# Performance work log

Measured on AMD Instinct MI355X. Metric: run time of the kernel, lower is better.

The kernel has to match this reference:

```python
import jax, jax.numpy as jnp
import numpy as np

B = 2048          # batch
K = 32            # max active features per side
NF = 22528        # feature_set.num_features
L1 = 2048
L2 = 16
L3 = 32
P = 8             # num_psqt_buckets
NLS = 8           # num_ls_buckets
QP = 255.0        # 8-bit unsigned LSQ upper bound


def setup_inputs() -> dict:
    key = jax.random.key(0)
    ks = jax.random.split(key, 16)
    us = jax.random.bernoulli(ks[0], 0.5, (B, 1)).astype(jnp.float32)
    them = 1.0 - us
    white_indices = jax.random.randint(ks[1], (B, K), 0, NF)
    black_indices = jax.random.randint(ks[2], (B, K), 0, NF)
    white_values = jnp.ones((B, K), jnp.float32)
    black_values = jnp.ones((B, K), jnp.float32)
    psqt_indices = jax.random.randint(ks[3], (B,), 0, P)
    layer_stack_indices = jax.random.randint(ks[4], (B,), 0, NLS)
    # parameters
    ft_weight = jax.random.normal(ks[5], (NF, L1 + P), jnp.float32) * 0.01
    ft_bias = jax.random.normal(ks[6], (L1 + P,), jnp.float32) * 0.01
    lsq_s = jnp.full((4,), 1.0 / 128.0, jnp.float32)  # per-group step size
    W1 = jax.random.normal(ks[7], (NLS, L2, L1), jnp.float32) * (1.0 / np.sqrt(L1))
    b1 = jnp.zeros((NLS, L2), jnp.float32)
    W2 = jax.random.normal(ks[8], (NLS, L3, L2), jnp.float32) * (1.0 / np.sqrt(L2))
    b2 = jnp.zeros((NLS, L3), jnp.float32)
    Wo = jax.random.normal(ks[9], (NLS, 1, L3), jnp.float32) * (1.0 / np.sqrt(L3))
    bo = jnp.zeros((NLS, 1), jnp.float32)
    return dict(us=us, them=them, white_indices=white_indices, white_values=white_values,
                black_indices=black_indices, black_values=black_values,
                psqt_indices=psqt_indices, layer_stack_indices=layer_stack_indices,
                ft_weight=ft_weight, ft_bias=ft_bias, lsq_s=lsq_s,
                W1=W1, b1=b1, W2=W2, b2=b2, Wo=Wo, bo=bo)


def _feature_transform(idx, val, ft_weight, ft_bias):
    # sparse accumulation: sum_k val[b,k] * ft_weight[idx[b,k], :]
    emb = ft_weight[idx]                           # [B, K, L1+P]
    return jnp.einsum('bk,bkd->bd', val, emb) + ft_bias


def _lsq(x, s):
    # LSQ activation, 4 groups over feature dim, 8-bit unsigned, STE round
    b, d = x.shape
    g = x.reshape(b, 4, d // 4) / s[None, :, None]
    gc = jnp.clip(g, 0.0, QP)
    gq = gc + jax.lax.stop_gradient(jnp.round(gc) - gc)
    return (gq * s[None, :, None]).reshape(b, d)


def reference(us, them, white_indices, white_values, black_indices, black_values,
              psqt_indices, layer_stack_indices,
              ft_weight, ft_bias, lsq_s, W1, b1, W2, b2, Wo, bo):
    wp = _feature_transform(white_indices, white_values, ft_weight, ft_bias)
    bp = _feature_transform(black_indices, black_values, ft_weight, ft_bias)
    w, wpsqt = wp[:, :L1], wp[:, L1:]
    b, bpsqt = bp[:, :L1], bp[:, L1:]
    l0 = us * jnp.concatenate([w, b], axis=1) + them * jnp.concatenate([b, w], axis=1)
    l0q = _lsq(l0, lsq_s)                          # [B, 2*L1]
    s0, s1, s2, s3 = jnp.split(l0q, 4, axis=1)
    l0_mixed = jnp.concatenate([s0 * s1, s2 * s3], axis=1)   # [B, L1]
    # psqt bucket gather
    wps = jnp.take_along_axis(wpsqt, psqt_indices[:, None], axis=1)  # [B,1]
    bps = jnp.take_along_axis(bpsqt, psqt_indices[:, None], axis=1)
    # per-sample layer-stack (expert) selection
    i = layer_stack_indices
    h1 = jnp.clip(jnp.einsum('bi,boi->bo', l0_mixed, W1[i]) + b1[i], 0.0, 1.0)
    h2 = jnp.clip(jnp.einsum('bi,boi->bo', h1, W2[i]) + b2[i], 0.0, 1.0)
    ls_out = jnp.einsum('bi,boi->bo', h2, Wo[i]) + bo[i]     # [B,1]
    return ls_out + (wps - bps) * (us - 0.5)
```

## Files before the change

### kernel.cpp

```cpp
#include <hip/hip_runtime.h>

#define BB 2048
#define K 32
#define ROW 2056
#define L1D 2048
#define NFEAT 22528

typedef unsigned short us8 __attribute__((ext_vector_type(8)));
typedef signed char    c8  __attribute__((ext_vector_type(8)));
typedef signed char    c16 __attribute__((ext_vector_type(16)));
typedef float          f8  __attribute__((ext_vector_type(8)));

#define S_T   (0.0625f / 128.0f)
#define INV_S (128.0f / 0.0625f)

#define TBLC_BYTES ((size_t)NFEAT * 2048)
#define W1_ELEMS   ((size_t)8 * 16 * L1D)
#define W1_OFF     TBLC_BYTES
#define PSQ_OFF    (W1_OFF + W1_ELEMS * 2)
#define WS_NEEDED  (PSQ_OFF + (size_t)NFEAT * 8 * 4)

#define TBL_N8 (NFEAT * 256)
#define W1_N8  ((int)(W1_ELEMS / 8))
#define CONV_N (TBL_N8 + W1_N8 + NFEAT)

__device__ __forceinline__ float bf2f(unsigned short s) {
    union { unsigned int u; float f; } v; v.u = ((unsigned int)s) << 16; return v.f;
}

__device__ __forceinline__ unsigned short f2bf(float f) {
    union { float f; unsigned int u; } v; v.f = f;
    const unsigned int u = v.u;
    return (unsigned short)((u + 0x7fffu + ((u >> 16) & 1u)) >> 16);
}

__device__ __forceinline__ signed char f2i8(float f) {
    return (signed char)(int)rintf(fminf(fmaxf(f * INV_S, -127.f), 127.f));
}

__device__ __forceinline__ void fma4(float4& a, float v, const float4 t) {
    a.x = fmaf(v, t.x, a.x); a.y = fmaf(v, t.y, a.y);
    a.z = fmaf(v, t.z, a.z); a.w = fmaf(v, t.w, a.w);
}

__device__ __forceinline__ float4 add4(float4 a, float4 b) {
    float4 r; r.x = a.x + b.x; r.y = a.y + b.y; r.z = a.z + b.z; r.w = a.w + b.w;
    return r;
}

__device__ __forceinline__ float4 mix4(float ua, float4 a, float ub, float4 b) {
    float4 r;
    r.x = fmaf(ua, a.x, ub * b.x); r.y = fmaf(ua, a.y, ub * b.y);
    r.z = fmaf(ua, a.z, ub * b.z); r.w = fmaf(ua, a.w, ub * b.w);
    return r;
}

__device__ __forceinline__ float lsq1(float g, float s) {
    return rintf(fminf(fmaxf(g / s, 0.f), 255.f)) * s;
}

__device__ __forceinline__ float4 lsq4(float4 g, float s) {
    float4 r;
    r.x = lsq1(g.x, s); r.y = lsq1(g.y, s); r.z = lsq1(g.z, s); r.w = lsq1(g.w, s);
    return r;
}

__device__ __forceinline__ float4 mul4(float4 a, float4 b) {
    float4 r; r.x = a.x * b.x; r.y = a.y * b.y; r.z = a.z * b.z; r.w = a.w * b.w;
    return r;
}

__global__ __launch_bounds__(256) void conv_all(const float* __restrict__ ftw,
                                                const float* __restrict__ W1,
                                                signed char* __restrict__ tblc,
                                                unsigned short* __restrict__ w1bf,
                                                float* __restrict__ psqtc) {
    int i = blockIdx.x * blockDim.x + threadIdx.x;
    const int stride = gridDim.x * blockDim.x;
    for (; i < CONV_N; i += stride) {
        if (i < TBL_N8) {
            const int row = i >> 8, c = i & 255;
            const float* src = ftw + (size_t)row * ROW + c * 8;
            const float4 a = ((const float4*)src)[0];
            const float4 b = ((const float4*)src)[1];
            c8 o;
            o[0] = f2i8(a.x); o[1] = f2i8(a.y); o[2] = f2i8(a.z); o[3] = f2i8(a.w);
            o[4] = f2i8(b.x); o[5] = f2i8(b.y); o[6] = f2i8(b.z); o[7] = f2i8(b.w);
            *(c8*)(tblc + ((size_t)row << 11) + c * 8) = o;
        } else if (i < TBL_N8 + W1_N8) {
            const int j = i - TBL_N8;
            const float* src = W1 + (size_t)j * 8;
            const float4 a = ((const float4*)src)[0];
            const float4 b = ((const float4*)src)[1];
            us8 o;
            o[0] = f2bf(a.x); o[1] = f2bf(a.y); o[2] = f2bf(a.z); o[3] = f2bf(a.w);
            o[4] = f2bf(b.x); o[5] = f2bf(b.y); o[6] = f2bf(b.z); o[7] = f2bf(b.w);
            *(us8*)(w1bf + (size_t)j * 8) = o;
        } else {
            const int r = i - TBL_N8 - W1_N8;
            const float4* src = (const float4*)(ftw + (size_t)r * ROW + 2048);
            float4* dst = (float4*)(psqtc + (size_t)r * 8);
            dst[0] = src[0]; dst[1] = src[1];
        }
    }
}

struct __align__(32) SBuf {
    float aw[2048];
    float ab[2048];
    float h1t[16];
    float h1[16];
    float h2[32];
    float psq;
};

__global__ __launch_bounds__(256, 4) void nnue_main2(
    const float* __restrict__ us_p, const float* __restrict__ them_p,
    const int* __restrict__ widx, const float* __restrict__ wval,
    const int* __restrict__ bidx, const float* __restrict__ bval,
    const int* __restrict__ psqt_idx, const int* __restrict__ ls_idx,
    const float* __restrict__ ftb, const float* __restrict__ lsq_s,
    const signed char* __restrict__ tblc, const unsigned short* __restrict__ w1bf,
    const float* __restrict__ psqtc,
    const float* __restrict__ b1, const float* __restrict__ W2,
    const float* __restrict__ b2, const float* __restrict__ Wo,
    const float* __restrict__ bo, float* __restrict__ out)
{
    __shared__ SBuf sb;
    const int b = blockIdx.x;
    const int t = threadIdx.x;

    const float usv = us_p[b];
    const float thv = them_p[b];

    const int side = t >> 7;
    const int tc   = t & 127;
    const int*   idxp = side ? bidx : widx;
    const float* valp = side ? bval : wval;
    const int kb = b * K;

    float acc[16];
    #pragma unroll
    for (int j = 0; j < 16; ++j) acc[j] = 0.f;

    c16 buf[8];
    #pragma unroll
    for (int p = 0; p < 8; ++p)
        buf[p] = ((const c16*)(tblc + ((size_t)idxp[kb + p] << 11)))[tc];
    #pragma unroll
    for (int k = 0; k < K; ++k) {
        const c16 l = buf[k & 7];
        if (k + 8 < K)
            buf[k & 7] = ((const c16*)(tblc + ((size_t)idxp[kb + k + 8] << 11)))[tc];
        const float v = valp[kb + k];
        #pragma unroll
        for (int j = 0; j < 16; ++j) acc[j] = fmaf(v, (float)l[j], acc[j]);
    }

    {
        float* dst = (side ? sb.ab : sb.aw) + 16 * tc;
        const float* fb = ftb + 16 * tc;
        #pragma unroll
        for (int j = 0; j < 16; ++j) dst[j] = fmaf(acc[j], S_T, fb[j]);
    }

    const int pi = psqt_idx[b];
    if (t < 64) {
        const int k = t & 31;
        const int   idx = (t < 32) ? widx[kb + k] : bidx[kb + k];
        const float val = (t < 32) ? wval[kb + k] : bval[kb + k];
        float c = val * psqtc[(size_t)idx * 8 + pi];
        c += __shfl_down(c, 16, 32); c += __shfl_down(c, 8, 32);
        c += __shfl_down(c, 4, 32);  c += __shfl_down(c, 2, 32);
        c += __shfl_down(c, 1, 32);
        const float bsum = __shfl(c, 32);
        if (t == 0) sb.psq = (c - bsum) * (usv - 0.5f);
    }
    __syncthreads();

    {
        const float s0 = lsq_s[0], s1 = lsq_s[1], s2 = lsq_s[2], s3 = lsq_s[3];
        const f8 aw = ((const f8*)sb.aw)[t];
        const f8 ab = ((const f8*)sb.ab)[t];
        const float sA = (t < 128) ? s0 : s1;
        const float sB = (t < 128) ? s2 : s3;
        f8 qa, qb;
        #pragma unroll
        for (int j = 0; j < 8; ++j) {
            qa[j] = lsq1(fmaf(usv, aw[j], thv * ab[j]), sA);
            qb[j] = lsq1(fmaf(usv, ab[j], thv * aw[j]), sB);
        }
        ((f8*)sb.aw)[t] = qa;
        ((f8*)sb.ab)[t] = qb;
    }
    __syncthreads();

    if (t < 128) {
        const f8 x = ((const f8*)sb.aw)[t];
        const f8 y = ((const f8*)sb.aw)[t + 128];
        ((f8*)sb.aw)[t] = x * y;
    } else {
        const f8 x = ((const f8*)sb.ab)[t - 128];
        const f8 y = ((const f8*)sb.ab)[t];
        ((f8*)sb.ab)[t - 128] = x * y;
    }
    __syncthreads();

    const int i = ls_idx[b];
    {
        const int o   = t >> 4;
        const int sub = t & 15;
        const us8* Wrow = (const us8*)(w1bf + (((size_t)i * 16 + o) << 11));
        f8 a8 = (f8)0.f;
        #pragma unroll
        for (int jj = 0; jj < 8; ++jj) {
            const int c = sub + (jj << 4);
            const f8 m = ((const f8*)sb.aw)[c];
            const us8 w = Wrow[c];
            #pragma unroll
            for (int j = 0; j < 8; ++j) a8[j] = fmaf(m[j], bf2f(w[j]), a8[j]);
        }
        #pragma unroll
        for (int jj = 8; jj < 16; ++jj) {
            const int c = sub + ((jj - 8) << 4);
            const f8 m = ((const f8*)sb.ab)[c];
            const us8 w = Wrow[sub + (jj << 4)];
            #pragma unroll
            for (int j = 0; j < 8; ++j) a8[j] = fmaf(m[j], bf2f(w[j]), a8[j]);
        }
        float acc1 = ((a8[0]+a8[1]) + (a8[2]+a8[3])) + ((a8[4]+a8[5]) + (a8[6]+a8[7]));
        acc1 += __shfl_down(acc1, 8, 16); acc1 += __shfl_down(acc1, 4, 16);
        acc1 += __shfl_down(acc1, 2, 16); acc1 += __shfl_down(acc1, 1, 16);
        if (sub == 0) sb.h1t[o] = acc1;
    }
    __syncthreads();

    if (t < 16) {
        const float v = sb.h1t[t] + b1[i * 16 + t];
        sb.h1[t] = fminf(fmaxf(v, 0.f), 1.f);
    }
    __syncthreads();

    if (t < 32) {
        const float* W2i = W2 + (size_t)i * 32 * 16 + t * 16;
        float v = b2[i * 32 + t];
        #pragma unroll
        for (int j = 0; j < 16; ++j) v = fmaf(sb.h1[j], W2i[j], v);
        sb.h2[t] = fminf(fmaxf(v, 0.f), 1.f);
    }
    __syncthreads();

    if (t == 0) {
        const float* Woi = Wo + (size_t)i * 32;
        float v = bo[i];
        #pragma unroll
        for (int j = 0; j < 32; ++j) v = fmaf(sb.h2[j], Woi[j], v);
        out[b] = v + sb.psq;
    }
}

__global__ __launch_bounds__(512, 4) void nnue_fwd_f32(
    const float* __restrict__ us_p, const float* __restrict__ them_p,
    const int* __restrict__ widx, const float* __restrict__ wval,
    const int* __restrict__ bidx, const float* __restrict__ bval,
    const int* __restrict__ psqt_idx, const int* __restrict__ ls_idx,
    const float* __restrict__ ftw, const float* __restrict__ ftb,
    const float* __restrict__ lsq_s, const float* __restrict__ W1,
    const float* __restrict__ b1, const float* __restrict__ W2,
    const float* __restrict__ b2, const float* __restrict__ Wo,
    const float* __restrict__ bo, float* __restrict__ out)
{
    const int b = blockIdx.x;
    const int t = threadIdx.x;
    __shared__ float4 sQA[512]; __shared__ float4 sQB[512]; __shared__ float4 sMx[512];
    __shared__ float sH1t[16]; __shared__ float sH1[16]; __shared__ float sH2[32];
    __shared__ float sPsq;
    const float usv = us_p[b]; const float thv = them_p[b];
    float4 aw = {0,0,0,0}, ab = {0,0,0,0};
    #pragma unroll 4
    for (int k = 0; k < K; ++k) {
        const int iw = widx[b*K+k]; const float vw = wval[b*K+k];
        const int ibx = bidx[b*K+k]; const float vb = bval[b*K+k];
        fma4(aw, vw, ((const float4*)(ftw + (size_t)iw * ROW))[t]);
        fma4(ab, vb, ((const float4*)(ftw + (size_t)ibx * ROW))[t]);
    }
    const int pi = psqt_idx[b];
    if (t < 64) {
        const int k = t & 31;
        const int   idx = (t < 32) ? widx[b*K+k] : bidx[b*K+k];
        const float val = (t < 32) ? wval[b*K+k] : bval[b*K+k];
        float cc = val * ftw[(size_t)idx * ROW + 2048 + pi];
        cc += __shfl_down(cc, 16, 32); cc += __shfl_down(cc, 8, 32);
        cc += __shfl_down(cc, 4, 32); cc += __shfl_down(cc, 2, 32); cc += __shfl_down(cc, 1, 32);
        const float bsum = __shfl(cc, 32);
        if (t == 0) sPsq = (cc - bsum) * (usv - 0.5f);
    }
    const float s0 = lsq_s[0], s1 = lsq_s[1], s2 = lsq_s[2], s3 = lsq_s[3];
    const float4 bias = ((const float4*)ftb)[t];
    aw = add4(aw, bias); ab = add4(ab, bias);
    const float sA = (t < 256) ? s0 : s1;
    const float sB = (t < 256) ? s2 : s3;
    sQA[t] = lsq4(mix4(usv, aw, thv, ab), sA);
    sQB[t] = lsq4(mix4(usv, ab, thv, aw), sB);
    __syncthreads();
    if (t < 256) { sMx[t] = mul4(sQA[t], sQA[t+256]); sMx[t+256] = mul4(sQB[t], sQB[t+256]); }
    __syncthreads();
    const int i = ls_idx[b];
    const float* W1i = W1 + (size_t)i * 16 * L1D;
    {
        const int o = t >> 5; const int sub = t & 31;
        const float4* Wrow = (const float4*)(W1i + o * L1D);
        float4 a4 = {0,0,0,0};
        #pragma unroll
        for (int jj = 0; jj < 16; ++jj) {
            const int j4 = sub + (jj << 5);
            const float4 m = sMx[j4]; const float4 w = Wrow[j4];
            a4.x = fmaf(m.x, w.x, a4.x); a4.y = fmaf(m.y, w.y, a4.y);
            a4.z = fmaf(m.z, w.z, a4.z); a4.w = fmaf(m.w, w.w, a4.w);
        }
        float acc = (a4.x + a4.y) + (a4.z + a4.w);
        acc += __shfl_down(acc, 16, 32); acc += __shfl_down(acc, 8, 32);
        acc += __shfl_down(acc, 4, 32); acc += __shfl_down(acc, 2, 32); acc += __shfl_down(acc, 1, 32);
        if (sub == 0) sH1t[o] = acc;
    }
    __syncthreads();
    if (t < 16) sH1[t] = fminf(fmaxf(sH1t[t] + b1[i*16+t], 0.f), 1.f);
    __syncthreads();
    if (t < 32) {
        const float* W2i = W2 + (size_t)i * 32 * 16 + t * 16;
        float v = b2[i*32+t];
        #pragma unroll
        for (int j = 0; j < 16; ++j) v = fmaf(sH1[j], W2i[j], v);
        sH2[t] = fminf(fmaxf(v, 0.f), 1.f);
    }
    __syncthreads();
    if (t == 0) {
        const float* Woi = Wo + (size_t)i * 32;
        float v = bo[i];
        #pragma unroll
        for (int j = 0; j < 32; ++j) v = fmaf(sH2[j], Woi[j], v);
        out[b] = v + sPsq;
    }
}

extern "C" void kernel_launch(void* const* d_in, const int* in_sizes, int n_in,
                              void* d_out, int out_size, void* d_ws, size_t ws_size,
                              hipStream_t stream) {
    const float* us_p  = (const float*)d_in[0];
    const float* them  = (const float*)d_in[1];
    const int*   widx  = (const int*)d_in[2];
    const float* wval  = (const float*)d_in[3];
    const int*   bidx  = (const int*)d_in[4];
    const float* bval  = (const float*)d_in[5];
    const int*   pidx  = (const int*)d_in[6];
    const int*   lidx  = (const int*)d_in[7];
    const float* ftw   = (const float*)d_in[8];
    const float* ftb   = (const float*)d_in[9];
    const float* lsqs  = (const float*)d_in[10];
    const float* W1    = (const float*)d_in[11];
    const float* b1    = (const float*)d_in[12];
    const float* W2    = (const float*)d_in[13];
    const float* b2    = (const float*)d_in[14];
    const float* Wo    = (const float*)d_in[15];
    const float* bo    = (const float*)d_in[16];
    float* out = (float*)d_out;

    if (ws_size >= WS_NEEDED) {
        signed char*    tblc  = (signed char*)d_ws;
        unsigned short* w1bf  = (unsigned short*)((char*)d_ws + W1_OFF);
        float*          psqtc = (float*)((char*)d_ws + PSQ_OFF);
        conv_all<<<dim3(8192), dim3(256), 0, stream>>>(ftw, W1, tblc, w1bf, psqtc);
        nnue_main2<<<dim3(BB), dim3(256), 0, stream>>>(
            us_p, them, widx, wval, bidx, bval, pidx, lidx,
            ftb, lsqs, tblc, w1bf, psqtc, b1, W2, b2, Wo, bo, out);
    } else {
        nnue_fwd_f32<<<dim3(BB), dim3(512), 0, stream>>>(
            us_p, them, widx, wval, bidx, bval, pidx, lidx,
            ftw, ftb, lsqs, W1, b1, W2, b2, Wo, bo, out);
    }
}
```

Baseline: 338.5 us.

## Split feature gather into column-tiled kernel with transposed int8 table

The int8 feature table is re-laid out as 16 column tiles of 128 bytes per feature. A new gather kernel assigns blocks to (tile, sample chunk) pairs, so each block touches only one 2.9 MB tile slice, which aims to improve cache locality of the random row gathers. The accumulators go through global fp32 scratch (2×16 MB) and are read back by a second kernel that does bias, LSQ and the layer stack. This adds an extra kernel launch and round-trip global traffic in exchange for the better gather locality.

```diff
diff --git a/kernel.cpp b/kernel.cpp
--- a/kernel.cpp
+++ b/kernel.cpp
@@ -5,6 +5,8 @@
 #define ROW 2056
 #define L1D 2048
 #define NFEAT 22528
+#define NTILE 16
+#define TCOLS 128
 
 typedef unsigned short us8 __attribute__((ext_vector_type(8)));
 typedef signed char    c8  __attribute__((ext_vector_type(8)));
@@ -14,15 +16,17 @@
 #define S_T   (0.0625f / 128.0f)
 #define INV_S (128.0f / 0.0625f)
 
-#define TBLC_BYTES ((size_t)NFEAT * 2048)
+#define TBLT_BYTES ((size_t)NFEAT * 2048)
 #define W1_ELEMS   ((size_t)8 * 16 * L1D)
-#define W1_OFF     TBLC_BYTES
+#define W1_OFF     TBLT_BYTES
 #define PSQ_OFF    (W1_OFF + W1_ELEMS * 2)
-#define WS_NEEDED  (PSQ_OFF + (size_t)NFEAT * 8 * 4)
-
-#define TBL_N8 (NFEAT * 256)
-#define W1_N8  ((int)(W1_ELEMS / 8))
-#define CONV_N (TBL_N8 + W1_N8 + NFEAT)
+#define ACCW_OFF   (PSQ_OFF + (size_t)NFEAT * 8 * 4)
+#define ACCB_OFF   (ACCW_OFF + (size_t)BB * L1D * 4)
+#define WS_NEEDED  (ACCB_OFF + (size_t)BB * L1D * 4)
+
+#define TBL_N8  (NFEAT * 256)
+#define W1_N8   ((int)(W1_ELEMS / 8))
+#define CONV_N  (TBL_N8 + W1_N8 + NFEAT)
 
 __device__ __forceinline__ float bf2f(unsigned short s) {
     union { unsigned int u; float f; } v; v.u = ((unsigned int)s) << 16; return v.f;
@@ -72,7 +76,7 @@
 
 __global__ __launch_bounds__(256) void conv_all(const float* __restrict__ ftw,
                                                 const float* __restrict__ W1,
-                                                signed char* __restrict__ tblc,
+                                                signed char* __restrict__ tblT,
                                                 unsigned short* __restrict__ w1bf,
                                                 float* __restrict__ psqtc) {
     int i = blockIdx.x * blockDim.x + threadIdx.x;
@@ -86,7 +90,8 @@
             c8 o;
             o[0] = f2i8(a.x); o[1] = f2i8(a.y); o[2] = f2i8(a.z); o[3] = f2i8(a.w);
             o[4] = f2i8(b.x); o[5] = f2i8(b.y); o[6] = f2i8(b.z); o[7] = f2i8(b.w);
-            *(c8*)(tblc + ((size_t)row << 11) + c * 8) = o;
+            signed char* dst = tblT + ((size_t)(c >> 4) * NFEAT + row) * TCOLS + (c & 15) * 8;
+            *(c8*)dst = o;
         } else if (i < TBL_N8 + W1_N8) {
             const int j = i - TBL_N8;
             const float* src = W1 + (size_t)j * 8;
@@ -105,6 +110,47 @@
     }
 }
 
+__global__ __launch_bounds__(256, 4) void gather_tiled(
+    const signed char* __restrict__ tblT,
+    const int* __restrict__ widx, const float* __restrict__ wval,
+    const int* __restrict__ bidx, const float* __restrict__ bval,
+    float* __restrict__ accW, float* __restrict__ accB)
+{
+    const int bid  = blockIdx.x;
+    const int tile = ((bid & 7) << 1) | ((bid >> 3) & 1);
+    const int chunk = bid >> 4;
+    const int t = threadIdx.x;
+    const int g = t >> 3;
+    const int lane = t & 7;
+    const int side = g >> 4;
+    const int s = chunk * 16 + (g & 15);
+
+    const int*   idxp = side ? bidx : widx;
+    const float* valp = side ? bval : wval;
+    const int kb = s * K;
+    const signed char* slice = tblT + (size_t)tile * NFEAT * TCOLS + lane * 16;
+
+    float acc[16];
+    #pragma unroll
+    for (int j = 0; j < 16; ++j) acc[j] = 0.f;
+
+    #pragma unroll 4
+    for (int k = 0; k < K; ++k) {
+        const int   f = idxp[kb + k];
+        const float v = valp[kb + k];
+        const c16 l = *(const c16*)(slice + (size_t)f * TCOLS);
+        #pragma unroll
+        for (int j = 0; j < 16; ++j) acc[j] = fmaf(v, (float)l[j], acc[j]);
+    }
+
+    float* dst = (side ? accB : accW) + (size_t)s * L1D + tile * TCOLS + lane * 16;
+    f8 lo, hi;
+    #pragma unroll
+    for (int j = 0; j < 8; ++j) { lo[j] = acc[j]; hi[j] = acc[j + 8]; }
+    ((f8*)dst)[0] = lo;
+    ((f8*)dst)[1] = hi;
+}
+
 struct __align__(32) SBuf {
     float aw[2048];
     float ab[2048];
@@ -114,14 +160,14 @@
     float psq;
 };
 
-__global__ __launch_bounds__(256, 4) void nnue_main2(
+__global__ __launch_bounds__(256, 4) void phase2(
     const float* __restrict__ us_p, const float* __restrict__ them_p,
     const int* __restrict__ widx, const float* __restrict__ wval,
     const int* __restrict__ bidx, const float* __restrict__ bval,
     const int* __restrict__ psqt_idx, const int* __restrict__ ls_idx,
     const float* __restrict__ ftb, const float* __restrict__ lsq_s,
-    const signed char* __restrict__ tblc, const unsigned short* __restrict__ w1bf,
-    const float* __restrict__ psqtc,
+    const float* __restrict__ accW, const float* __restrict__ accB,
+    const unsigned short* __restrict__ w1bf, const float* __restrict__ psqtc,
     const float* __restrict__ b1, const float* __restrict__ W2,
     const float* __restrict__ b2, const float* __restrict__ Wo,
     const float* __restrict__ bo, float* __restrict__ out)
@@ -129,40 +175,27 @@
     __shared__ SBuf sb;
     const int b = blockIdx.x;
     const int t = threadIdx.x;
+    const int kb = b * K;
 
     const float usv = us_p[b];
     const float thv = them_p[b];
 
-    const int side = t >> 7;
-    const int tc   = t & 127;
-    const int*   idxp = side ? bidx : widx;
-    const float* valp = side ? bval : wval;
-    const int kb = b * K;
-
-    float acc[16];
+    const f8 awr = *(const f8*)(accW + (size_t)b * L1D + t * 8);
+    const f8 abr = *(const f8*)(accB + (size_t)b * L1D + t * 8);
+    const f8 fb8 = ((const f8*)ftb)[t];
+    const float s0 = lsq_s[0], s1 = lsq_s[1], s2 = lsq_s[2], s3 = lsq_s[3];
+    const float sA = (t < 128) ? s0 : s1;
+    const float sB = (t < 128) ? s2 : s3;
+    f8 qa, qb;
     #pragma unroll
-    for (int j = 0; j < 16; ++j) acc[j] = 0.f;
-
-    c16 buf[8];
-    #pragma unroll
-    for (int p = 0; p < 8; ++p)
-        buf[p] = ((const c16*)(tblc + ((size_t)idxp[kb + p] << 11)))[tc];
-    #pragma unroll
-    for (int k = 0; k < K; ++k) {
-        const c16 l = buf[k & 7];
-        if (k + 8 < K)
-            buf[k & 7] = ((const c16*)(tblc + ((size_t)idxp[kb + k + 8] << 11)))[tc];
-        const float v = valp[kb + k];
-        #pragma unroll
-        for (int j = 0; j < 16; ++j) acc[j] = fmaf(v, (float)l[j], acc[j]);
-    }
-
-    {
-        float* dst = (side ? sb.ab : sb.aw) + 16 * tc;
-        const float* fb = ftb + 16 * tc;
-        #pragma unroll
-        for (int j = 0; j < 16; ++j) dst[j] = fmaf(acc[j], S_T, fb[j]);
-    }
+    for (int j = 0; j < 8; ++j) {
+        const float aw = fmaf(awr[j], S_T, fb8[j]);
+        const float ab = fmaf(abr[j], S_T, fb8[j]);
+        qa[j] = lsq1(fmaf(usv, aw, thv * ab), sA);
+        qb[j] = lsq1(fmaf(usv, ab, thv * aw), sB);
+    }
+    ((f8*)sb.aw)[t] = qa;
+    ((f8*)sb.ab)[t] = qb;
 
     const int pi = psqt_idx[b];
     if (t < 64) {
@@ -175,23 +208,6 @@
         c += __shfl_down(c, 1, 32);
         const float bsum = __shfl(c, 32);
         if (t == 0) sb.psq = (c - bsum) * (usv - 0.5f);
-    }
-    __syncthreads();
-
-    {
-        const float s0 = lsq_s[0], s1 = lsq_s[1], s2 = lsq_s[2], s3 = lsq_s[3];
-        const f8 aw = ((const f8*)sb.aw)[t];
-        const f8 ab = ((const f8*)sb.ab)[t];
-        const float sA = (t < 128) ? s0 : s1;
-        const float sB = (t < 128) ? s2 : s3;
-        f8 qa, qb;
-        #pragma unroll
-        for (int j = 0; j < 8; ++j) {
-            qa[j] = lsq1(fmaf(usv, aw[j], thv * ab[j]), sA);
-            qb[j] = lsq1(fmaf(usv, ab[j], thv * aw[j]), sB);
-        }
-        ((f8*)sb.aw)[t] = qa;
-        ((f8*)sb.ab)[t] = qb;
     }
     __syncthreads();
 
@@ -366,13 +382,17 @@
     float* out = (float*)d_out;
 
     if (ws_size >= WS_NEEDED) {
-        signed char*    tblc  = (signed char*)d_ws;
+        signed char*    tblT  = (signed char*)d_ws;
         unsigned short* w1bf  = (unsigned short*)((char*)d_ws + W1_OFF);
         float*          psqtc = (float*)((char*)d_ws + PSQ_OFF);
-        conv_all<<<dim3(8192), dim3(256), 0, stream>>>(ftw, W1, tblc, w1bf, psqtc);
-        nnue_main2<<<dim3(BB), dim3(256), 0, stream>>>(
+        float*          accW  = (float*)((char*)d_ws + ACCW_OFF);
+        float*          accB  = (float*)((char*)d_ws + ACCB_OFF);
+        conv_all<<<dim3(8192), dim3(256), 0, stream>>>(ftw, W1, tblT, w1bf, psqtc);
+        gather_tiled<<<dim3(2048), dim3(256), 0, stream>>>(
+            tblT, widx, wval, bidx, bval, accW, accB);
+        phase2<<<dim3(BB), dim3(256), 0, stream>>>(
             us_p, them, widx, wval, bidx, bval, pidx, lidx,
-            ftb, lsqs, tblc, w1bf, psqtc, b1, W2, b2, Wo, bo, out);
+            ftb, lsqs, accW, accB, w1bf, psqtc, b1, W2, b2, Wo, bo, out);
     } else {
         nnue_fwd_f32<<<dim3(BB), dim3(512), 0, stream>>>(
             us_p, them, widx, wval, bidx, bval, pidx, lidx,
```

After: 343.0 us. About the same (+1.3%).
